# Kernel optimization log

Measured on AMD Instinct MI355X. Metric: run time of the kernel, lower is better.

The kernel has to match this reference:

```python
import jax, jax.numpy as jnp
import numpy as np

IN_F = 4096
OUT_F = 11008
GROUP_SIZE = 128
NUM_GROUPS = (IN_F + GROUP_SIZE - 1) // GROUP_SIZE  # 32
N_HIGH = int(OUT_F * 0.25)   # 2752
N_LOW = OUT_F - N_HIGH       # 8256
B, S = 2, 2048


def setup_inputs() -> dict:
    key = jax.random.key(0)
    ks = jax.random.split(key, 9)
    x = jax.random.normal(ks[0], (B, S, IN_F), dtype=jnp.float32)
    # INT8 symmetric codes for high-precision columns
    high_prec_weight = jax.random.randint(ks[1], (IN_F, N_HIGH), -128, 128, dtype=jnp.int32)
    # per-group, per-column scales (positive, realistic magnitude)
    high_prec_scales = jax.random.uniform(ks[2], (NUM_GROUPS, N_HIGH), jnp.float32, 1e-4, 2e-2)
    # 4-bit asymmetric codes in [0, 15]
    low_prec_weight = jax.random.randint(ks[3], (IN_F, N_LOW), 0, 16, dtype=jnp.int32)
    low_prec_scales = jax.random.uniform(ks[4], (IN_F, 1), jnp.float32, 1e-4, 2e-2)
    low_prec_scales2 = jax.random.uniform(ks[5], (1, N_LOW), jnp.float32, 0.5, 2.0)
    low_prec_zeros = jnp.round(jax.random.uniform(ks[6], (IN_F, 1), jnp.float32, 0.0, 15.0))
    # inverse column permutation restoring original order
    col_indices_inv = jax.random.permutation(ks[7], OUT_F).astype(jnp.int64)
    bias = jax.random.normal(ks[8], (OUT_F,), dtype=jnp.float32) * 0.02
    return {
        "x": x,
        "high_prec_weight": high_prec_weight,
        "high_prec_scales": high_prec_scales,
        "low_prec_weight": low_prec_weight,
        "low_prec_scales": low_prec_scales,
        "low_prec_scales2": low_prec_scales2,
        "low_prec_zeros": low_prec_zeros,
        "col_indices_inv": col_indices_inv,
        "bias": bias,
    }


def _dequantize(high_w, high_scales, low_w, low_s1, low_s2, low_z, col_inv):
    # High: group-wise symmetric INT8 dequant. K divisible by GROUP_SIZE here (no pad).
    w_high = (high_w.astype(jnp.float32)
              .reshape(NUM_GROUPS, GROUP_SIZE, N_HIGH)
              * high_scales[:, None, :]).reshape(IN_F, N_HIGH)
    # Low: SINQ dual-scale asymmetric dequant: ((q - z) * s1) * s2
    w_low = (low_w.astype(jnp.float32) - low_z) * low_s1 * low_s2
    # Reassemble original column order: W_kn [in_features, out_features]
    w = jnp.concatenate([w_high, w_low], axis=1)[:, col_inv]
    return w


def reference(x, high_prec_weight, high_prec_scales, low_prec_weight,
              low_prec_scales, low_prec_scales2, low_prec_zeros,
              col_indices_inv, bias):
    w_kn = _dequantize(high_prec_weight, high_prec_scales, low_prec_weight,
                       low_prec_scales, low_prec_scales2, low_prec_zeros,
                       col_indices_inv)
    # F.linear(x, W_original) with W_original = w_kn.T  ->  x @ w_kn
    out = jnp.einsum('bsk,kn->bsn', x, w_kn) + bias
    return out
```

## Files before the change

### kernel.cpp

```cpp
#include <hip/hip_runtime.h>
#include <hip/hip_bf16.h>

#define IN_F   4096
#define OUT_F  11008
#define NHIGH  2752
#define NLOW   8256
#define M_TOT  4096

typedef __attribute__((ext_vector_type(8))) short bf16x8;
typedef __attribute__((ext_vector_type(4))) float f32x4;
typedef __attribute__((ext_vector_type(4))) float f32x4v;

__device__ __forceinline__ short f2bf(float f) {
    union { float f; unsigned u; } v; v.f = f;
    unsigned r = (v.u + 0x7fffu + ((v.u >> 16) & 1u)) >> 16;
    return (short)(r & 0xffffu);
}

__device__ __forceinline__ void async16(const void* g, const void* l) {
    __builtin_amdgcn_global_load_lds(
        (const __attribute__((address_space(1))) unsigned int*)g,
        (__attribute__((address_space(3))) unsigned int*)l, 16, 0, 0);
}

__global__ void fwd_perm_kernel(const int* __restrict__ cinv, int* __restrict__ fwd) {
    int n = blockIdx.x * blockDim.x + threadIdx.x;
    if (n < OUT_F) fwd[cinv[n]] = n;
}

__global__ void cvt_x_kernel(const float* __restrict__ x, short* __restrict__ xb) {
    const int nv = (M_TOT * IN_F) / 8;
    for (int i = blockIdx.x * blockDim.x + threadIdx.x; i < nv;
         i += gridDim.x * blockDim.x) {
        const f32x4v* p = (const f32x4v*)(x + (long)i * 8);
        f32x4v a = __builtin_nontemporal_load(p);
        f32x4v b = __builtin_nontemporal_load(p + 1);
        bf16x8 o;
        o[0] = f2bf(a[0]); o[1] = f2bf(a[1]); o[2] = f2bf(a[2]); o[3] = f2bf(a[3]);
        o[4] = f2bf(b[0]); o[5] = f2bf(b[1]); o[6] = f2bf(b[2]); o[7] = f2bf(b[3]);
        *(bf16x8*)(xb + (long)i * 8) = o;
    }
}

__global__ void dequant_kernel(const int* __restrict__ hw, const float* __restrict__ hs,
                               const int* __restrict__ lw, const float* __restrict__ s1,
                               const float* __restrict__ s2, const float* __restrict__ zp,
                               const int* __restrict__ fwd,
                               short* __restrict__ wt) {
    __shared__ short tile[64 * 66];
    const int t  = threadIdx.x;
    const int c0 = blockIdx.x * 64;
    const int k0 = blockIdx.y * 64;
    const int cl = t & 63;
    const int w  = t >> 6;

    if (c0 < NHIGH) {
        const int ci = c0 + cl;
        #pragma unroll
        for (int i = 0; i < 16; ++i) {
            const int kl = w + 4 * i;
            const int k  = k0 + kl;
            int   q   = __builtin_nontemporal_load(&hw[(long)k * NHIGH + ci]);
            float val = (float)q * hs[(k >> 7) * NHIGH + ci];
            tile[cl * 66 + kl] = f2bf(val);
        }
    } else {
        const int ci = c0 - NHIGH + cl;
        const float s2v = s2[ci];
        #pragma unroll
        for (int i = 0; i < 16; ++i) {
            const int kl = w + 4 * i;
            const int k  = k0 + kl;
            int   q   = __builtin_nontemporal_load(&lw[(long)k * NLOW + ci]);
            float val = ((float)q - zp[k]) * s1[k] * s2v;
            tile[cl * 66 + kl] = f2bf(val);
        }
    }
    __syncthreads();
    const int oc = t >> 2;
    const int kq = (t & 3) * 16;
    bf16x8 o0, o1;
    #pragma unroll
    for (int j = 0; j < 8; ++j) {
        o0[j] = tile[oc * 66 + kq + j];
        o1[j] = tile[oc * 66 + kq + 8 + j];
    }
    const int ndst = fwd[c0 + oc];
    short* dst = wt + (long)ndst * IN_F + k0 + kq;
    *(bf16x8*)dst       = o0;
    *(bf16x8*)(dst + 8) = o1;
}

#define BM 128
#define BN 128
#define BK 64
#define KT (IN_F / BK)
#define NTIL (OUT_F / BN)
#define MTIL (M_TOT / BM)
#define NWG3 (NTIL * MTIL)

#define BAR()    __builtin_amdgcn_s_barrier()
#define VMC0()   asm volatile("s_waitcnt vmcnt(0)" ::: "memory")

__global__ __launch_bounds__(256, 2) void gemm_kernel(
    const short* __restrict__ A,
    const short* __restrict__ Bt,
    const float* __restrict__ bias,
    float* __restrict__ C) {
    __shared__ __align__(16) short lds_s[32768];
    char* const lds = (char*)lds_s;

    const int t    = threadIdx.x;
    const int lane = t & 63;
    const int w    = t >> 6;
    const int wr   = w >> 1;
    const int wc   = w & 1;

    const int swz   = (blockIdx.x % 8) * (NWG3 / 8) + blockIdx.x / 8;
    const int sr    = swz / (8 * NTIL);
    const int in_sr = swz % (8 * NTIL);
    const int nb    = in_sr / 8;
    const int mb    = sr * 8 + (in_sr & 7);
    const int m0    = mb * BM;
    const int n0    = nb * BN;

    const int srow = w * 32 + (lane >> 3);
    const int scb  = ((lane & 7) ^ (lane >> 3)) * 16;
    const char* gA0 = (const char*)A  + (long)(m0 + srow) * (IN_F * 2) + scb;
    const char* gB0 = (const char*)Bt + (long)(n0 + srow) * (IN_F * 2) + scb;

    const int rl  = (lane & 15) * 128;
    const int kb0 = ((lane >> 4) * 16) ^ ((lane & 7) << 4);
    const int kb1 = kb0 ^ 64;

#define STAGE_TILE(buf, ktile) do {                                              \
        const char* _ga = gA0 + (ktile) * 128;                                   \
        const char* _gb = gB0 + (ktile) * 128;                                   \
        char* _la = lds + (buf) * 32768 +         w * 4096 + (lane) * 16;        \
        char* _lb = lds + (buf) * 32768 + 16384 + w * 4096 + (lane) * 16;        \
        _Pragma("unroll")                                                        \
        for (int _j = 0; _j < 4; ++_j) {                                         \
            async16(_ga + (long)(_j * 8) * (IN_F * 2), _la + _j * 1024);         \
            async16(_gb + (long)(_j * 8) * (IN_F * 2), _lb + _j * 1024);         \
        }                                                                        \
    } while (0)

    f32x4 acc[4][4];
    #pragma unroll
    for (int i = 0; i < 4; ++i)
        #pragma unroll
        for (int j = 0; j < 4; ++j)
            acc[i][j] = (f32x4){0.f, 0.f, 0.f, 0.f};

    bf16x8 af[4][2], bfm[4][2];

#define RD_ALL(buf) do {                                                         \
        char* _pa = lds + (buf) * 32768 +         (wr * 64) * 128 + rl;          \
        char* _pb = lds + (buf) * 32768 + 16384 + (wc * 64) * 128 + rl;          \
        _Pragma("unroll")                                                        \
        for (int _i = 0; _i < 4; ++_i) {                                         \
            af[_i][0]  = *(const bf16x8*)(_pa + _i * 2048 + kb0);                \
            af[_i][1]  = *(const bf16x8*)(_pa + _i * 2048 + kb1);                \
            bfm[_i][0] = *(const bf16x8*)(_pb + _i * 2048 + kb0);                \
            bfm[_i][1] = *(const bf16x8*)(_pb + _i * 2048 + kb1);                \
        }                                                                        \
    } while (0)

#define TILE_BODY(buf, ktn) do {                                                 \
        RD_ALL(buf);                                                             \
        STAGE_TILE((buf) ^ 1, ktn);                                              \
        __builtin_amdgcn_s_setprio(1);                                           \
        _Pragma("unroll")                                                        \
        for (int _m = 0; _m < 4; ++_m)                                           \
        _Pragma("unroll")                                                        \
        for (int _n = 0; _n < 4; ++_n) {                                         \
            acc[_m][_n] = __builtin_amdgcn_mfma_f32_16x16x32_bf16(               \
                af[_m][0], bfm[_n][0], acc[_m][_n], 0, 0, 0);                    \
            acc[_m][_n] = __builtin_amdgcn_mfma_f32_16x16x32_bf16(               \
                af[_m][1], bfm[_n][1], acc[_m][_n], 0, 0, 0);                    \
        }                                                                        \
        __builtin_amdgcn_s_setprio(0);                                           \
        VMC0(); BAR();                                                           \
    } while (0)

    STAGE_TILE(0, 0);
    VMC0();
    BAR();

    #pragma unroll 1
    for (int it = 0; it < KT / 2; ++it) {
        const int kt1 = 2 * it + 1;
        const int kt2 = (2 * it + 2 < KT) ? 2 * it + 2 : KT - 1;
        TILE_BODY(0, kt1);
        TILE_BODY(1, kt2);
    }

    const int er = m0 + wr * 64 + (lane >> 4) * 4;
    const int ec = n0 + wc * 64 + (lane & 15);
    #pragma unroll
    for (int ni = 0; ni < 4; ++ni) {
        const float bv = bias[ec + ni * 16];
        #pragma unroll
        for (int mi = 0; mi < 4; ++mi) {
            #pragma unroll
            for (int r = 0; r < 4; ++r) {
                __builtin_nontemporal_store(
                    acc[mi][ni][r] + bv,
                    &C[(long)(er + mi * 16 + r) * OUT_F + ec + ni * 16]);
            }
        }
    }
}

extern "C" void kernel_launch(void* const* d_in, const int* in_sizes, int n_in,
                              void* d_out, int out_size, void* d_ws, size_t ws_size,
                              hipStream_t stream) {
    const float* x    = (const float*)d_in[0];
    const int*   hw   = (const int*)d_in[1];
    const float* hs   = (const float*)d_in[2];
    const int*   lw   = (const int*)d_in[3];
    const float* s1   = (const float*)d_in[4];
    const float* s2   = (const float*)d_in[5];
    const float* zp   = (const float*)d_in[6];
    const int*   cinv = (const int*)d_in[7];
    const float* bias = (const float*)d_in[8];
    float*       out  = (float*)d_out;

    short* wt  = (short*)d_ws;
    short* xb  = (short*)((char*)d_ws + (size_t)OUT_F * IN_F * 2);
    int*   fwd = (int*)((char*)d_ws + (size_t)OUT_F * IN_F * 2
                                    + (size_t)M_TOT * IN_F * 2);

    fwd_perm_kernel<<<(OUT_F + 255) / 256, 256, 0, stream>>>(cinv, fwd);
    cvt_x_kernel<<<2048, 256, 0, stream>>>(x, xb);
    dequant_kernel<<<dim3(OUT_F / 64, IN_F / 64), 256, 0, stream>>>(
        hw, hs, lw, s1, s2, zp, fwd, wt);
    gemm_kernel<<<NWG3, 256, 0, stream>>>(xb, wt, bias, out);
}
```

Before: 416.0 us.

## Store activations k-tile-major and load A fragments from global straight into registers

The x-to-bf16 conversion now writes activations in a k-tile-major layout, so each MFMA A fragment is a contiguous 16-byte load. The GEMM stops staging A through LDS. Each wave prefetches its A fragments for the next k-tile into a second register set while the MFMAs run on the current one, and only B still goes through LDS double buffering. This removes the LDS traffic and bank pressure for A. In exchange, the two waves that share A rows both fetch them from global/L2, register use rises, and the LDS allocation grows even though less LDS is used.

```diff
diff --git a/kernel.cpp b/kernel.cpp
--- a/kernel.cpp
+++ b/kernel.cpp
@@ -28,17 +28,21 @@
     if (n < OUT_F) fwd[cinv[n]] = n;
 }
 
-__global__ void cvt_x_kernel(const float* __restrict__ x, short* __restrict__ xb) {
+__global__ void cvt_x_kernel(const float* __restrict__ x, short* __restrict__ xb2) {
     const int nv = (M_TOT * IN_F) / 8;
-    for (int i = blockIdx.x * blockDim.x + threadIdx.x; i < nv;
-         i += gridDim.x * blockDim.x) {
-        const f32x4v* p = (const f32x4v*)(x + (long)i * 8);
+    for (int v = blockIdx.x * blockDim.x + threadIdx.x; v < nv;
+         v += gridDim.x * blockDim.x) {
+        const f32x4v* p = (const f32x4v*)(x + (long)v * 8);
         f32x4v a = __builtin_nontemporal_load(p);
         f32x4v b = __builtin_nontemporal_load(p + 1);
         bf16x8 o;
         o[0] = f2bf(a[0]); o[1] = f2bf(a[1]); o[2] = f2bf(a[2]); o[3] = f2bf(a[3]);
         o[4] = f2bf(b[0]); o[5] = f2bf(b[1]); o[6] = f2bf(b[2]); o[7] = f2bf(b[3]);
-        *(bf16x8*)(xb + (long)i * 8) = o;
+        const int m  = v >> 9;
+        const int k8 = v & 511;
+        const int kt = k8 >> 3;
+        const int ko = (k8 & 7) * 8;
+        *(bf16x8*)(xb2 + (long)kt * 262144 + m * 64 + ko) = o;
     }
 }
 
@@ -103,11 +107,11 @@
 #define VMC0()   asm volatile("s_waitcnt vmcnt(0)" ::: "memory")
 
 __global__ __launch_bounds__(256, 2) void gemm_kernel(
-    const short* __restrict__ A,
+    const short* __restrict__ A2,
     const short* __restrict__ Bt,
     const float* __restrict__ bias,
     float* __restrict__ C) {
-    __shared__ __align__(16) short lds_s[32768];
+    __shared__ __align__(16) short lds_s[40960];
     char* const lds = (char*)lds_s;
 
     const int t    = threadIdx.x;
@@ -126,22 +130,38 @@
 
     const int srow = w * 32 + (lane >> 3);
     const int scb  = ((lane & 7) ^ (lane >> 3)) * 16;
-    const char* gA0 = (const char*)A  + (long)(m0 + srow) * (IN_F * 2) + scb;
     const char* gB0 = (const char*)Bt + (long)(n0 + srow) * (IN_F * 2) + scb;
+
+    const char* gA2 = (const char*)A2
+        + (long)(m0 + wr * 64 + (lane & 15)) * 128 + (lane >> 4) * 16;
 
     const int rl  = (lane & 15) * 128;
     const int kb0 = ((lane >> 4) * 16) ^ ((lane & 7) << 4);
     const int kb1 = kb0 ^ 64;
 
-#define STAGE_TILE(buf, ktile) do {                                              \
-        const char* _ga = gA0 + (ktile) * 128;                                   \
+#define STAGE_B(buf, ktile) do {                                                 \
         const char* _gb = gB0 + (ktile) * 128;                                   \
-        char* _la = lds + (buf) * 32768 +         w * 4096 + (lane) * 16;        \
-        char* _lb = lds + (buf) * 32768 + 16384 + w * 4096 + (lane) * 16;        \
-        _Pragma("unroll")                                                        \
-        for (int _j = 0; _j < 4; ++_j) {                                         \
-            async16(_ga + (long)(_j * 8) * (IN_F * 2), _la + _j * 1024);         \
+        char* _lb = lds + (buf) * 16384 + w * 4096 + lane * 16;                  \
+        _Pragma("unroll")                                                        \
+        for (int _j = 0; _j < 4; ++_j)                                           \
             async16(_gb + (long)(_j * 8) * (IN_F * 2), _lb + _j * 1024);         \
+    } while (0)
+
+#define PREF_A(areg, ktn) do {                                                   \
+        const char* _pa = gA2 + (long)(ktn) * 524288;                            \
+        _Pragma("unroll")                                                        \
+        for (int _mi = 0; _mi < 4; ++_mi)                                        \
+        _Pragma("unroll")                                                        \
+        for (int _kk = 0; _kk < 2; ++_kk)                                        \
+            areg[_mi][_kk] = *(const bf16x8*)(_pa + _mi * 2048 + _kk * 64);      \
+    } while (0)
+
+#define RD_B(buf) do {                                                           \
+        char* _pb = lds + (buf) * 16384 + wc * 8192 + rl;                        \
+        _Pragma("unroll")                                                        \
+        for (int _n = 0; _n < 4; ++_n) {                                         \
+            bfm[_n][0] = *(const bf16x8*)(_pb + _n * 2048 + kb0);                \
+            bfm[_n][1] = *(const bf16x8*)(_pb + _n * 2048 + kb1);                \
         }                                                                        \
     } while (0)
 
@@ -152,38 +172,28 @@
         for (int j = 0; j < 4; ++j)
             acc[i][j] = (f32x4){0.f, 0.f, 0.f, 0.f};
 
-    bf16x8 af[4][2], bfm[4][2];
-
-#define RD_ALL(buf) do {                                                         \
-        char* _pa = lds + (buf) * 32768 +         (wr * 64) * 128 + rl;          \
-        char* _pb = lds + (buf) * 32768 + 16384 + (wc * 64) * 128 + rl;          \
-        _Pragma("unroll")                                                        \
-        for (int _i = 0; _i < 4; ++_i) {                                         \
-            af[_i][0]  = *(const bf16x8*)(_pa + _i * 2048 + kb0);                \
-            af[_i][1]  = *(const bf16x8*)(_pa + _i * 2048 + kb1);                \
-            bfm[_i][0] = *(const bf16x8*)(_pb + _i * 2048 + kb0);                \
-            bfm[_i][1] = *(const bf16x8*)(_pb + _i * 2048 + kb1);                \
-        }                                                                        \
-    } while (0)
-
-#define TILE_BODY(buf, ktn) do {                                                 \
-        RD_ALL(buf);                                                             \
-        STAGE_TILE((buf) ^ 1, ktn);                                              \
+    bf16x8 aA[4][2], aB[4][2], bfm[4][2];
+
+#define TILE_BODY(buf, aU, aP, ktn) do {                                         \
+        PREF_A(aP, ktn);                                                         \
+        STAGE_B((buf) ^ 1, ktn);                                                 \
+        RD_B(buf);                                                               \
         __builtin_amdgcn_s_setprio(1);                                           \
         _Pragma("unroll")                                                        \
         for (int _m = 0; _m < 4; ++_m)                                           \
         _Pragma("unroll")                                                        \
         for (int _n = 0; _n < 4; ++_n) {                                         \
             acc[_m][_n] = __builtin_amdgcn_mfma_f32_16x16x32_bf16(               \
-                af[_m][0], bfm[_n][0], acc[_m][_n], 0, 0, 0);                    \
+                aU[_m][0], bfm[_n][0], acc[_m][_n], 0, 0, 0);                    \
             acc[_m][_n] = __builtin_amdgcn_mfma_f32_16x16x32_bf16(               \
-                af[_m][1], bfm[_n][1], acc[_m][_n], 0, 0, 0);                    \
+                aU[_m][1], bfm[_n][1], acc[_m][_n], 0, 0, 0);                    \
         }                                                                        \
         __builtin_amdgcn_s_setprio(0);                                           \
         VMC0(); BAR();                                                           \
     } while (0)
 
-    STAGE_TILE(0, 0);
+    PREF_A(aA, 0);
+    STAGE_B(0, 0);
     VMC0();
     BAR();
 
@@ -191,8 +201,8 @@
     for (int it = 0; it < KT / 2; ++it) {
         const int kt1 = 2 * it + 1;
         const int kt2 = (2 * it + 2 < KT) ? 2 * it + 2 : KT - 1;
-        TILE_BODY(0, kt1);
-        TILE_BODY(1, kt2);
+        TILE_BODY(0, aA, aB, kt1);
+        TILE_BODY(1, aB, aA, kt2);
     }
 
     const int er = m0 + wr * 64 + (lane >> 4) * 4;
@@ -227,13 +237,13 @@
     float*       out  = (float*)d_out;
 
     short* wt  = (short*)d_ws;
-    short* xb  = (short*)((char*)d_ws + (size_t)OUT_F * IN_F * 2);
+    short* xb2 = (short*)((char*)d_ws + (size_t)OUT_F * IN_F * 2);
     int*   fwd = (int*)((char*)d_ws + (size_t)OUT_F * IN_F * 2
                                     + (size_t)M_TOT * IN_F * 2);
 
     fwd_perm_kernel<<<(OUT_F + 255) / 256, 256, 0, stream>>>(cinv, fwd);
-    cvt_x_kernel<<<2048, 256, 0, stream>>>(x, xb);
+    cvt_x_kernel<<<2048, 256, 0, stream>>>(x, xb2);
     dequant_kernel<<<dim3(OUT_F / 64, IN_F / 64), 256, 0, stream>>>(
         hw, hs, lw, s1, s2, zp, fwd, wt);
-    gemm_kernel<<<NWG3, 256, 0, stream>>>(xb, wt, bias, out);
-}
+    gemm_kernel<<<NWG3, 256, 0, stream>>>(xb2, wt, bias, out);
+}
```

New measurement: 823.1 us. 97.9% more time.

## Split GEMM into bf16 high columns and int8 W4A8 low columns

Applied to the files above, without the earlier changes.

The low-precision columns are now computed with an int8 MFMA GEMM instead of bf16. Activations are multiplied by s1 and quantized per row to int8 with a dynamic scale, and weights are stored as int8 (q minus rounded zero-point). The s2 and row scales are applied in the epilogue. Dequantized weights are grouped into separate high and low buffers rather than permuted into original order, using scan-built tables, and the epilogue scatters outputs through the permutation. This halves weight and activation bytes and doubles MFMA throughput for 75% of the columns. The cost is extra activation quantization error, an assumption that zero-points are integers, and uncoalesced permuted output stores.

```diff
diff --git a/kernel.cpp b/kernel.cpp
--- a/kernel.cpp
+++ b/kernel.cpp
@@ -6,10 +6,12 @@
 #define NHIGH  2752
 #define NLOW   8256
 #define M_TOT  4096
+#define NHP    2816
+#define NLP    8320
 
 typedef __attribute__((ext_vector_type(8))) short bf16x8;
 typedef __attribute__((ext_vector_type(4))) float f32x4;
-typedef __attribute__((ext_vector_type(4))) float f32x4v;
+typedef __attribute__((ext_vector_type(4))) int   i32x4;
 
 __device__ __forceinline__ short f2bf(float f) {
     union { float f; unsigned u; } v; v.f = f;
@@ -23,31 +25,94 @@
         (__attribute__((address_space(3))) unsigned int*)l, 16, 0, 0);
 }
 
-__global__ void fwd_perm_kernel(const int* __restrict__ cinv, int* __restrict__ fwd) {
-    int n = blockIdx.x * blockDim.x + threadIdx.x;
-    if (n < OUT_F) fwd[cinv[n]] = n;
-}
-
-__global__ void cvt_x_kernel(const float* __restrict__ x, short* __restrict__ xb) {
-    const int nv = (M_TOT * IN_F) / 8;
-    for (int i = blockIdx.x * blockDim.x + threadIdx.x; i < nv;
-         i += gridDim.x * blockDim.x) {
-        const f32x4v* p = (const f32x4v*)(x + (long)i * 8);
-        f32x4v a = __builtin_nontemporal_load(p);
-        f32x4v b = __builtin_nontemporal_load(p + 1);
-        bf16x8 o;
-        o[0] = f2bf(a[0]); o[1] = f2bf(a[1]); o[2] = f2bf(a[2]); o[3] = f2bf(a[3]);
-        o[4] = f2bf(b[0]); o[5] = f2bf(b[1]); o[6] = f2bf(b[2]); o[7] = f2bf(b[3]);
-        *(bf16x8*)(xb + (long)i * 8) = o;
+__global__ void t1_count(const int* __restrict__ cinv, int* __restrict__ bcnt) {
+    __shared__ int wtot[4];
+    const int t = threadIdx.x, n = blockIdx.x * 256 + t, w = t >> 6;
+    int f = (cinv[n] < NHIGH) ? 1 : 0;
+    unsigned long long mask = __ballot(f);
+    if ((t & 63) == 0) wtot[w] = __popcll(mask);
+    __syncthreads();
+    if (t == 0) bcnt[blockIdx.x] = wtot[0] + wtot[1] + wtot[2] + wtot[3];
+}
+
+__global__ void t2_scan(const int* __restrict__ bcnt, int* __restrict__ boff) {
+    const int lane = threadIdx.x;
+    int v = (lane < 43) ? bcnt[lane] : 0;
+    int s = v;
+    #pragma unroll
+    for (int i = 1; i < 64; i <<= 1) { int u = __shfl_up(s, i); if (lane >= i) s += u; }
+    if (lane < 43) boff[lane] = s - v;
+}
+
+__global__ void t3_tables(const int* __restrict__ cinv, const int* __restrict__ boff,
+                          int* __restrict__ rbs, int* __restrict__ och,
+                          int* __restrict__ ocl, float* __restrict__ scl,
+                          const float* __restrict__ s2) {
+    __shared__ int wtot[4];
+    const int t = threadIdx.x, n = blockIdx.x * 256 + t;
+    const int lane = t & 63, w = t >> 6;
+    const int c = cinv[n];
+    const int f = (c < NHIGH) ? 1 : 0;
+    unsigned long long mask = __ballot(f);
+    int wpre = __popcll(mask & ((1ull << lane) - 1ull));
+    if (lane == 63) wtot[w] = wpre + f;
+    __syncthreads();
+    int off = 0;
+    for (int i = 0; i < w; ++i) off += wtot[i];
+    const int H = boff[blockIdx.x] + off + wpre;
+    const int r = f ? H : (n - H);
+    rbs[c] = r;
+    if (f) { och[r] = n; }
+    else   { ocl[r] = n; scl[r] = s2[c - NHIGH]; }
+}
+
+__global__ void pad_kernel(signed char* __restrict__ wt8, short* __restrict__ wth,
+                           int* __restrict__ och, int* __restrict__ ocl) {
+    const int idx = blockIdx.x * 256 + threadIdx.x;
+    if (idx < 16384) {
+        ((int4*)(wt8 + (long)NLOW * IN_F))[idx] = make_int4(0, 0, 0, 0);
+    } else if (idx < 49152) {
+        ((int4*)((char*)wth + (long)NHIGH * IN_F * 2))[idx - 16384] = make_int4(0, 0, 0, 0);
+    }
+    if (idx < 64)  och[NHIGH + idx] = -1;
+    else if (idx < 128) ocl[NLOW + idx - 64] = -1;
+}
+
+__global__ void quant_kernel(const float* __restrict__ x, const float* __restrict__ s1,
+                             short* __restrict__ xb, signed char* __restrict__ xq,
+                             float* __restrict__ beta) {
+    const int t = threadIdx.x, lane = t & 63, w = t >> 6;
+    const int m = blockIdx.x * 4 + w;
+    const float* xr = x + (long)m * IN_F;
+    float v[64];
+    float amax = 0.f;
+    #pragma unroll
+    for (int j = 0; j < 64; ++j) {
+        const int k = j * 64 + lane;
+        float xv = xr[k];
+        xb[(long)m * IN_F + k] = f2bf(xv);
+        v[j] = xv * s1[k];
+        amax = fmaxf(amax, fabsf(v[j]));
+    }
+    #pragma unroll
+    for (int i = 1; i < 64; i <<= 1) amax = fmaxf(amax, __shfl_xor(amax, i));
+    const float inv = (amax > 0.f) ? 127.f / amax : 0.f;
+    if (lane == 0) beta[m] = (amax > 0.f) ? amax / 127.f : 0.f;
+    #pragma unroll
+    for (int j = 0; j < 64; ++j) {
+        const int k = j * 64 + lane;
+        int qi = (int)rintf(v[j] * inv);
+        qi = qi > 127 ? 127 : (qi < -127 ? -127 : qi);
+        xq[(long)m * IN_F + k] = (signed char)qi;
     }
 }
 
 __global__ void dequant_kernel(const int* __restrict__ hw, const float* __restrict__ hs,
-                               const int* __restrict__ lw, const float* __restrict__ s1,
-                               const float* __restrict__ s2, const float* __restrict__ zp,
-                               const int* __restrict__ fwd,
-                               short* __restrict__ wt) {
+                               const int* __restrict__ lw, const float* __restrict__ zp,
+                               const int* __restrict__ rbs,
+                               short* __restrict__ wth, signed char* __restrict__ wt8) {
     __shared__ short tile[64 * 66];
+    __shared__ signed char t8[64 * 68];
     const int t  = threadIdx.x;
     const int c0 = blockIdx.x * 64;
     const int k0 = blockIdx.y * 64;
@@ -60,55 +125,57 @@
         for (int i = 0; i < 16; ++i) {
             const int kl = w + 4 * i;
             const int k  = k0 + kl;
-            int   q   = __builtin_nontemporal_load(&hw[(long)k * NHIGH + ci]);
-            float val = (float)q * hs[(k >> 7) * NHIGH + ci];
-            tile[cl * 66 + kl] = f2bf(val);
-        }
+            int q = __builtin_nontemporal_load(&hw[(long)k * NHIGH + ci]);
+            tile[cl * 66 + kl] = f2bf((float)q * hs[(k >> 7) * NHIGH + ci]);
+        }
+        __syncthreads();
+        const int oc = t >> 2;
+        const int kq = (t & 3) * 16;
+        bf16x8 o0, o1;
+        #pragma unroll
+        for (int j = 0; j < 8; ++j) {
+            o0[j] = tile[oc * 66 + kq + j];
+            o1[j] = tile[oc * 66 + kq + 8 + j];
+        }
+        const int r = rbs[c0 + oc];
+        short* dst = wth + (long)r * IN_F + k0 + kq;
+        *(bf16x8*)dst       = o0;
+        *(bf16x8*)(dst + 8) = o1;
     } else {
         const int ci = c0 - NHIGH + cl;
-        const float s2v = s2[ci];
         #pragma unroll
         for (int i = 0; i < 16; ++i) {
             const int kl = w + 4 * i;
             const int k  = k0 + kl;
-            int   q   = __builtin_nontemporal_load(&lw[(long)k * NLOW + ci]);
-            float val = ((float)q - zp[k]) * s1[k] * s2v;
-            tile[cl * 66 + kl] = f2bf(val);
-        }
-    }
-    __syncthreads();
-    const int oc = t >> 2;
-    const int kq = (t & 3) * 16;
-    bf16x8 o0, o1;
-    #pragma unroll
-    for (int j = 0; j < 8; ++j) {
-        o0[j] = tile[oc * 66 + kq + j];
-        o1[j] = tile[oc * 66 + kq + 8 + j];
-    }
-    const int ndst = fwd[c0 + oc];
-    short* dst = wt + (long)ndst * IN_F + k0 + kq;
-    *(bf16x8*)dst       = o0;
-    *(bf16x8*)(dst + 8) = o1;
-}
-
-#define BM 128
-#define BN 128
-#define BK 64
-#define KT (IN_F / BK)
-#define NTIL (OUT_F / BN)
-#define MTIL (M_TOT / BM)
-#define NWG3 (NTIL * MTIL)
-
-#define BAR()    __builtin_amdgcn_s_barrier()
-#define VMC0()   asm volatile("s_waitcnt vmcnt(0)" ::: "memory")
+            int q  = __builtin_nontemporal_load(&lw[(long)k * NLOW + ci]);
+            int zi = (int)rintf(zp[k]);
+            t8[cl * 68 + kl] = (signed char)(q - zi);
+        }
+        __syncthreads();
+        const int oc = t >> 2;
+        const int kq = (t & 3) * 16;
+        union { signed char c[16]; int4 v; } u;
+        #pragma unroll
+        for (int j = 0; j < 16; ++j) u.c[j] = t8[oc * 68 + kq + j];
+        const int r = rbs[c0 + oc];
+        *(int4*)(wt8 + (long)r * IN_F + k0 + kq) = u.v;
+    }
+}
+
+#define HB   704
+#define LBK  2080
+#define NWG  (HB + LBK)
+
+#define BAR()   __builtin_amdgcn_s_barrier()
+#define VMC0()  asm volatile("s_waitcnt vmcnt(0)" ::: "memory")
 
 __global__ __launch_bounds__(256, 2) void gemm_kernel(
-    const short* __restrict__ A,
-    const short* __restrict__ Bt,
-    const float* __restrict__ bias,
-    float* __restrict__ C) {
-    __shared__ __align__(16) short lds_s[32768];
-    char* const lds = (char*)lds_s;
+    const short* __restrict__ xb, const short* __restrict__ wth,
+    const signed char* __restrict__ xq, const signed char* __restrict__ wt8,
+    const int* __restrict__ och, const int* __restrict__ ocl,
+    const float* __restrict__ scl, const float* __restrict__ beta,
+    const float* __restrict__ bias, float* __restrict__ out) {
+    __shared__ __align__(16) char lds[65536];
 
     const int t    = threadIdx.x;
     const int lane = t & 63;
@@ -116,45 +183,45 @@
     const int wr   = w >> 1;
     const int wc   = w & 1;
 
-    const int swz   = (blockIdx.x % 8) * (NWG3 / 8) + blockIdx.x / 8;
-    const int sr    = swz / (8 * NTIL);
-    const int in_sr = swz % (8 * NTIL);
-    const int nb    = in_sr / 8;
-    const int mb    = sr * 8 + (in_sr & 7);
-    const int m0    = mb * BM;
-    const int n0    = nb * BN;
+    const int swz = (blockIdx.x % 8) * (NWG / 8) + blockIdx.x / 8;
+    const int h0  = (swz * 22) / 87;
+    const int h1  = ((swz + 1) * 22) / 87;
+    const bool hi = (h1 > h0);
+    int mb, nb;
+    if (hi) { const int hb = h0;       const int in = hb % 176; nb = in / 8; mb = (hb / 176) * 8 + (in & 7); }
+    else    { const int lb = swz - h0; const int in = lb % 520; nb = in / 8; mb = (lb / 520) * 8 + (in & 7); }
+    const int m0 = mb * 128;
+    const int n0 = nb * 128;
 
     const int srow = w * 32 + (lane >> 3);
     const int scb  = ((lane & 7) ^ (lane >> 3)) * 16;
-    const char* gA0 = (const char*)A  + (long)(m0 + srow) * (IN_F * 2) + scb;
-    const char* gB0 = (const char*)Bt + (long)(n0 + srow) * (IN_F * 2) + scb;
-
     const int rl  = (lane & 15) * 128;
     const int kb0 = ((lane >> 4) * 16) ^ ((lane & 7) << 4);
     const int kb1 = kb0 ^ 64;
 
-#define STAGE_TILE(buf, ktile) do {                                              \
-        const char* _ga = gA0 + (ktile) * 128;                                   \
-        const char* _gb = gB0 + (ktile) * 128;                                   \
-        char* _la = lds + (buf) * 32768 +         w * 4096 + (lane) * 16;        \
-        char* _lb = lds + (buf) * 32768 + 16384 + w * 4096 + (lane) * 16;        \
+#define STAGE2(gA, gB, S, buf, kbyte) do {                                       \
+        const char* _ga = (gA) + (kbyte);                                        \
+        const char* _gb = (gB) + (kbyte);                                        \
+        char* _la = lds + (buf) * 32768 +         w * 4096 + lane * 16;          \
+        char* _lb = lds + (buf) * 32768 + 16384 + w * 4096 + lane * 16;          \
         _Pragma("unroll")                                                        \
         for (int _j = 0; _j < 4; ++_j) {                                         \
-            async16(_ga + (long)(_j * 8) * (IN_F * 2), _la + _j * 1024);         \
-            async16(_gb + (long)(_j * 8) * (IN_F * 2), _lb + _j * 1024);         \
-        }                                                                        \
-    } while (0)
-
-    f32x4 acc[4][4];
-    #pragma unroll
-    for (int i = 0; i < 4; ++i)
-        #pragma unroll
-        for (int j = 0; j < 4; ++j)
-            acc[i][j] = (f32x4){0.f, 0.f, 0.f, 0.f};
-
-    bf16x8 af[4][2], bfm[4][2];
-
-#define RD_ALL(buf) do {                                                         \
+            async16(_ga + (long)(_j * 8) * (S), _la + _j * 1024);                \
+            async16(_gb + (long)(_j * 8) * (S), _lb + _j * 1024);                \
+        }                                                                        \
+    } while (0)
+
+    if (hi) {
+        const char* gA = (const char*)xb  + (long)(m0 + srow) * 8192 + scb;
+        const char* gB = (const char*)wth + (long)(n0 + srow) * 8192 + scb;
+        f32x4 acc[4][4];
+        #pragma unroll
+        for (int i = 0; i < 4; ++i)
+            #pragma unroll
+            for (int j = 0; j < 4; ++j) acc[i][j] = (f32x4){0.f, 0.f, 0.f, 0.f};
+        bf16x8 af[4][2], bfm[4][2];
+
+#define RD_BF(buf) do {                                                          \
         char* _pa = lds + (buf) * 32768 +         (wr * 64) * 128 + rl;          \
         char* _pb = lds + (buf) * 32768 + 16384 + (wc * 64) * 128 + rl;          \
         _Pragma("unroll")                                                        \
@@ -166,9 +233,9 @@
         }                                                                        \
     } while (0)
 
-#define TILE_BODY(buf, ktn) do {                                                 \
-        RD_ALL(buf);                                                             \
-        STAGE_TILE((buf) ^ 1, ktn);                                              \
+#define TILE_BF(buf, ktn) do {                                                   \
+        RD_BF(buf);                                                              \
+        STAGE2(gA, gB, 8192, (buf) ^ 1, (long)(ktn) * 128);                      \
         __builtin_amdgcn_s_setprio(1);                                           \
         _Pragma("unroll")                                                        \
         for (int _m = 0; _m < 4; ++_m)                                           \
@@ -183,30 +250,98 @@
         VMC0(); BAR();                                                           \
     } while (0)
 
-    STAGE_TILE(0, 0);
-    VMC0();
-    BAR();
-
-    #pragma unroll 1
-    for (int it = 0; it < KT / 2; ++it) {
-        const int kt1 = 2 * it + 1;
-        const int kt2 = (2 * it + 2 < KT) ? 2 * it + 2 : KT - 1;
-        TILE_BODY(0, kt1);
-        TILE_BODY(1, kt2);
-    }
-
-    const int er = m0 + wr * 64 + (lane >> 4) * 4;
-    const int ec = n0 + wc * 64 + (lane & 15);
-    #pragma unroll
-    for (int ni = 0; ni < 4; ++ni) {
-        const float bv = bias[ec + ni * 16];
-        #pragma unroll
-        for (int mi = 0; mi < 4; ++mi) {
+        STAGE2(gA, gB, 8192, 0, 0);
+        VMC0(); BAR();
+        #pragma unroll 1
+        for (int it = 0; it < 32; ++it) {
+            const int kt1 = 2 * it + 1;
+            const int kt2 = (2 * it + 2 < 64) ? 2 * it + 2 : 63;
+            TILE_BF(0, kt1);
+            TILE_BF(1, kt2);
+        }
+        const int er  = m0 + wr * 64 + (lane >> 4) * 4;
+        const int ecr = n0 + wc * 64 + (lane & 15);
+        #pragma unroll
+        for (int ni = 0; ni < 4; ++ni) {
+            const int n = och[ecr + ni * 16];
+            if (n >= 0) {
+                const float bv = bias[n];
+                #pragma unroll
+                for (int mi = 0; mi < 4; ++mi)
+                    #pragma unroll
+                    for (int r = 0; r < 4; ++r)
+                        out[(long)(er + mi * 16 + r) * OUT_F + n] = acc[mi][ni][r] + bv;
+            }
+        }
+    } else {
+        const char* gA = (const char*)xq  + (long)(m0 + srow) * 4096 + scb;
+        const char* gB = (const char*)wt8 + (long)(n0 + srow) * 4096 + scb;
+        i32x4 acc[4][4];
+        #pragma unroll
+        for (int i = 0; i < 4; ++i)
             #pragma unroll
-            for (int r = 0; r < 4; ++r) {
-                __builtin_nontemporal_store(
-                    acc[mi][ni][r] + bv,
-                    &C[(long)(er + mi * 16 + r) * OUT_F + ec + ni * 16]);
+            for (int j = 0; j < 4; ++j) acc[i][j] = (i32x4){0, 0, 0, 0};
+        i32x4 ai[4][2], bi[4][2];
+
+#define RD_I8(buf) do {                                                          \
+        char* _pa = lds + (buf) * 32768 +         (wr * 64) * 128 + rl;          \
+        char* _pb = lds + (buf) * 32768 + 16384 + (wc * 64) * 128 + rl;          \
+        _Pragma("unroll")                                                        \
+        for (int _i = 0; _i < 4; ++_i) {                                         \
+            ai[_i][0] = *(const i32x4*)(_pa + _i * 2048 + kb0);                  \
+            ai[_i][1] = *(const i32x4*)(_pa + _i * 2048 + kb1);                  \
+            bi[_i][0] = *(const i32x4*)(_pb + _i * 2048 + kb0);                  \
+            bi[_i][1] = *(const i32x4*)(_pb + _i * 2048 + kb1);                  \
+        }                                                                        \
+    } while (0)
+
+#define TILE_I8(buf, ktn) do {                                                   \
+        RD_I8(buf);                                                              \
+        STAGE2(gA, gB, 4096, (buf) ^ 1, (long)(ktn) * 128);                      \
+        __builtin_amdgcn_s_setprio(1);                                           \
+        _Pragma("unroll")                                                        \
+        for (int _m = 0; _m < 4; ++_m)                                           \
+        _Pragma("unroll")                                                        \
+        for (int _n = 0; _n < 4; ++_n) {                                         \
+            acc[_m][_n] = __builtin_amdgcn_mfma_i32_16x16x64_i8(                 \
+                ai[_m][0], bi[_n][0], acc[_m][_n], 0, 0, 0);                     \
+            acc[_m][_n] = __builtin_amdgcn_mfma_i32_16x16x64_i8(                 \
+                ai[_m][1], bi[_n][1], acc[_m][_n], 0, 0, 0);                     \
+        }                                                                        \
+        __builtin_amdgcn_s_setprio(0);                                           \
+        VMC0(); BAR();                                                           \
+    } while (0)
+
+        STAGE2(gA, gB, 4096, 0, 0);
+        VMC0(); BAR();
+        #pragma unroll 1
+        for (int it = 0; it < 16; ++it) {
+            const int kt1 = 2 * it + 1;
+            const int kt2 = (2 * it + 2 < 32) ? 2 * it + 2 : 31;
+            TILE_I8(0, kt1);
+            TILE_I8(1, kt2);
+        }
+        const int er  = m0 + wr * 64 + (lane >> 4) * 4;
+        const int ecr = n0 + wc * 64 + (lane & 15);
+        float bt[4][4];
+        #pragma unroll
+        for (int mi = 0; mi < 4; ++mi)
+            #pragma unroll
+            for (int r = 0; r < 4; ++r)
+                bt[mi][r] = beta[er + mi * 16 + r];
+        #pragma unroll
+        for (int ni = 0; ni < 4; ++ni) {
+            const int rk = ecr + ni * 16;
+            const int n  = ocl[rk];
+            if (n >= 0) {
+                const float sc = scl[rk];
+                const float bv = bias[n];
+                #pragma unroll
+                for (int mi = 0; mi < 4; ++mi)
+                    #pragma unroll
+                    for (int r = 0; r < 4; ++r)
+                        out[(long)(er + mi * 16 + r) * OUT_F + n] =
+                            (float)acc[mi][ni][r] * bt[mi][r] * sc + bv;
             }
         }
     }
@@ -226,14 +361,25 @@
     const float* bias = (const float*)d_in[8];
     float*       out  = (float*)d_out;
 
-    short* wt  = (short*)d_ws;
-    short* xb  = (short*)((char*)d_ws + (size_t)OUT_F * IN_F * 2);
-    int*   fwd = (int*)((char*)d_ws + (size_t)OUT_F * IN_F * 2
-                                    + (size_t)M_TOT * IN_F * 2);
-
-    fwd_perm_kernel<<<(OUT_F + 255) / 256, 256, 0, stream>>>(cinv, fwd);
-    cvt_x_kernel<<<2048, 256, 0, stream>>>(x, xb);
-    dequant_kernel<<<dim3(OUT_F / 64, IN_F / 64), 256, 0, stream>>>(
-        hw, hs, lw, s1, s2, zp, fwd, wt);
-    gemm_kernel<<<NWG3, 256, 0, stream>>>(xb, wt, bias, out);
-}
+    char* p = (char*)d_ws;
+    signed char* wt8  = (signed char*)p;            p += (size_t)NLP * IN_F;
+    short*       wth  = (short*)p;                  p += (size_t)NHP * IN_F * 2;
+    signed char* xq   = (signed char*)p;            p += (size_t)M_TOT * IN_F;
+    short*       xb   = (short*)p;                  p += (size_t)M_TOT * IN_F * 2;
+    float*       beta = (float*)p;                  p += (size_t)M_TOT * 4;
+    int*         och  = (int*)p;                    p += (size_t)NHP * 4;
+    int*         ocl  = (int*)p;                    p += (size_t)NLP * 4;
+    float*       scl  = (float*)p;                  p += (size_t)NLP * 4;
+    int*         rbs  = (int*)p;                    p += (size_t)OUT_F * 4;
+    int*         bcnt = (int*)p;                    p += 64 * 4;
+    int*         boff = (int*)p;                    p += 64 * 4;
+
+    t1_count<<<43, 256, 0, stream>>>(cinv, bcnt);
+    t2_scan<<<1, 64, 0, stream>>>(bcnt, boff);
+    t3_tables<<<43, 256, 0, stream>>>(cinv, boff, rbs, och, ocl, scl, s2);
+    pad_kernel<<<192, 256, 0, stream>>>(wt8, wth, och, ocl);
+    quant_kernel<<<1024, 256, 0, stream>>>(x, s1, xb, xq, beta);
+    dequant_kernel<<<dim3(172, 64), 256, 0, stream>>>(hw, hs, lw, zp, rbs, wth, wt8);
+    gemm_kernel<<<NWG, 256, 0, stream>>>(xb, wth, xq, wt8, och, ocl, scl, beta,
+                                         bias, out);
+}
```

Result: slower. 509.7 us (+22.5%).
